# Performance work log

Hardware: AMD Instinct MI355X
Metric: run time of the kernel (lower is better)

The kernel has to match this reference:

```python
import jax, jax.numpy as jnp
import numpy as np

B, L, P, T, D, H = 16, 50, 49, 20, 512, 8
DH = D // H
DFF = 4 * D
EPS = 1e-6
NEG = -1000000000.0


def gelu_tanh(x):
    return 0.5 * x * (1.0 + jnp.tanh(jnp.sqrt(2.0 / jnp.pi) * (x + 0.044715 * x ** 3)))


def layernorm(x, a, b):
    # torch LayerNorm (custom): unbiased std, divide by (std + eps)
    mean = jnp.mean(x, axis=-1, keepdims=True)
    std = jnp.sqrt(jnp.var(x, axis=-1, keepdims=True, ddof=1))
    return a * (x - mean) / (std + EPS) + b


def setup_inputs() -> dict:
    key = jax.random.key(0)
    ks = jax.random.split(key, 20)
    s = 0.02
    return {
        "img": jax.random.normal(ks[0], (B, L, P, D), jnp.float32),
        "title": jax.random.normal(ks[1], (B, L, T, D), jnp.float32),
        "mask": jax.random.randint(ks[2], (B, L, T), 0, 2, jnp.int32),
        "scale_img": jax.random.normal(ks[3], (H, P), jnp.float32) * 0.1,
        "scale_title": jax.random.normal(ks[4], (H, T), jnp.float32) * 0.1,
        "w_proj": jax.random.normal(ks[5], (D, D), jnp.float32) * s,
        "b_proj": jnp.zeros((D,), jnp.float32),
        "w1_img": jax.random.normal(ks[6], (DFF, D), jnp.float32) * s,
        "b1_img": jnp.zeros((DFF,), jnp.float32),
        "w2_img": jax.random.normal(ks[7], (D, DFF), jnp.float32) * s,
        "b2_img": jnp.zeros((D,), jnp.float32),
        "w1_tit": jax.random.normal(ks[8], (DFF, D), jnp.float32) * s,
        "b1_tit": jnp.zeros((DFF,), jnp.float32),
        "w2_tit": jax.random.normal(ks[9], (D, DFF), jnp.float32) * s,
        "b2_tit": jnp.zeros((D,), jnp.float32),
        "ln_a_img": jnp.ones((D,), jnp.float32),
        "ln_b_img": jnp.zeros((D,), jnp.float32),
        "ln_a_tit": jnp.ones((D,), jnp.float32),
        "ln_b_tit": jnp.zeros((D,), jnp.float32),
    }


def _forward(img, title, mask, scale_img, scale_title, w_proj, b_proj,
             w1_img, b1_img, w2_img, b2_img, w1_tit, b1_tit, w2_tit, b2_tit,
             ln_a_img, ln_b_img, ln_a_tit, ln_b_tit):
    imgh = img.reshape(B, L, P, H, DH)      # [B,L,P,H,dh]
    tith = title.reshape(B, L, T, H, DH)    # [B,L,T,H,dh]

    raw = jnp.einsum('blphd,blthd->blhpt', imgh, tith) / jnp.sqrt(jnp.float32(DH))
    # corr_title is the transpose of the UNSCALED corr_img
    corr_img = raw * scale_img[None, None, :, :, None]                     # [B,L,H,P,T]
    corr_tit = jnp.swapaxes(raw, -1, -2) * scale_title[None, None, :, :, None]  # [B,L,H,T,P]

    m_img = mask[:, :, None, None, :]  # [B,L,1,1,T] -> broadcast over H,P
    m_tit = mask[:, :, None, :, None]  # [B,L,1,T,1]
    corr_img = jnp.where(m_img == 0, NEG, corr_img)
    corr_tit = jnp.where(m_tit == 0, NEG, corr_tit)

    p_img = jax.nn.softmax(corr_img, axis=-1)  # [B,L,H,P,T]
    p_tit = jax.nn.softmax(corr_tit, axis=-1)  # [B,L,H,T,P]

    # T != P, so the torch code takes the else branch (swapped outputs)
    hid_img = jnp.einsum('blhtp,blphd->blthd', p_tit, imgh).reshape(B, L, T, D)
    hid_tit = jnp.einsum('blhpt,blthd->blphd', p_img, tith).reshape(B, L, P, D)

    # both projected with img_layer (faithful to source)
    hid_img = hid_img @ w_proj.T + b_proj
    hid_tit = hid_tit @ w_proj.T + b_proj

    ffn_img = gelu_tanh(hid_img @ w1_img.T + b1_img) @ w2_img.T + b2_img
    ffn_tit = gelu_tanh(hid_tit @ w1_tit.T + b1_tit) @ w2_tit.T + b2_tit

    out_img = hid_img + layernorm(ffn_img, ln_a_img, ln_b_img)
    out_tit = hid_tit + layernorm(ffn_tit, ln_a_tit, ln_b_tit)
    return out_img, out_tit


def reference(img, title, mask, scale_img, scale_title, w_proj, b_proj,
              w1_img, b1_img, w2_img, b2_img, w1_tit, b1_tit, w2_tit, b2_tit,
              ln_a_img, ln_b_img, ln_a_tit, ln_b_tit):
    return _forward(img, title, mask, scale_img, scale_title, w_proj, b_proj,
                    w1_img, b1_img, w2_img, b2_img, w1_tit, b1_tit, w2_tit, b2_tit,
                    ln_a_img, ln_b_img, ln_a_tit, ln_b_tit)
```

## Files before the change

kernel.cpp:

```cpp
#include <hip/hip_runtime.h>
#include <hip/hip_bf16.h>

#define BB   16
#define LL   50
#define PP   49
#define TT   20
#define DD   512
#define HH   8
#define DHH  64
#define DFF  2048

#define BL     (BB*LL)
#define ROWS_I (BL*TT)
#define ROWS_T (BL*PP)
#define ROWS_A (ROWS_I+ROWS_T)
#define OUT_I_ELEMS ((size_t)ROWS_I*DD)
#define CHUNK 19600

#define R1_OFF 80281600ull
#define R2_OFF 136806400ull
#define R3_OFF 176947200ull

typedef __attribute__((ext_vector_type(8))) short bf16x8;
typedef __attribute__((ext_vector_type(4))) float f32x4;

__device__ __forceinline__ unsigned short f2bf(float f) {
    union { float f; unsigned int i; } w; w.f = f;
    unsigned int x = w.i;
    unsigned int r = (x + 0x7fffu + ((x >> 16) & 1u)) >> 16;
    return (unsigned short)r;
}
__device__ __forceinline__ float gelu_tanh_f(float x) {
    float c = 0.7978845608028654f * (x + 0.044715f * x * x * x);
    return 0.5f * x * (1.0f + tanhf(c));
}

__global__ __launch_bounds__(256) void cvt_kernel(
    const float* __restrict__ s, unsigned short* __restrict__ d, int n4)
{
    int i = blockIdx.x * 256 + threadIdx.x;
    if (i < n4) {
        float4 v = ((const float4*)s)[i];
        ushort4 u;
        u.x = f2bf(v.x); u.y = f2bf(v.y); u.z = f2bf(v.z); u.w = f2bf(v.w);
        ((ushort4*)d)[i] = u;
    }
}

__global__ __launch_bounds__(256) void attn_kernel(
    const float* __restrict__ img, const float* __restrict__ title,
    const int* __restrict__ mask, const float* __restrict__ scale_img,
    const float* __restrict__ scale_tit, unsigned short* __restrict__ hid)
{
    const int blh = blockIdx.x;
    const int h  = blh & 7;
    const int bl = blh >> 3;
    const int tid = threadIdx.x;

    __shared__ float simg[PP][DHH + 1];
    __shared__ float stit[TT][DHH + 1];
    __shared__ float S [PP][TT];
    __shared__ float pI[PP][TT];
    __shared__ float pT[TT][PP];
    __shared__ int   msk[TT];

    const float* imgbase = img   + (size_t)bl * PP * DD + h * DHH;
    const float* titbase = title + (size_t)bl * TT * DD + h * DHH;
    for (int i = tid; i < PP * DHH; i += 256) {
        int p = i >> 6, d = i & 63;
        simg[p][d] = imgbase[(size_t)p * DD + d];
    }
    for (int i = tid; i < TT * DHH; i += 256) {
        int t = i >> 6, d = i & 63;
        stit[t][d] = titbase[(size_t)t * DD + d];
    }
    if (tid < TT) msk[tid] = mask[bl * TT + tid];
    __syncthreads();

    for (int i = tid; i < PP * TT; i += 256) {
        int p = i / TT, t = i % TT;
        float s = 0.f;
        #pragma unroll 8
        for (int d = 0; d < DHH; ++d) s += simg[p][d] * stit[t][d];
        S[p][t] = s * 0.125f;
    }
    __syncthreads();

    if (tid < PP) {
        const int p = tid;
        const float sc = scale_img[h * PP + p];
        float m = -1e30f;
        #pragma unroll
        for (int t = 0; t < TT; ++t) {
            float x = (msk[t] == 0) ? -1e9f : S[p][t] * sc;
            m = fmaxf(m, x);
        }
        float sum = 0.f;
        #pragma unroll
        for (int t = 0; t < TT; ++t) {
            float x = (msk[t] == 0) ? -1e9f : S[p][t] * sc;
            float e = __expf(x - m);
            pI[p][t] = e; sum += e;
        }
        float inv = 1.f / sum;
        #pragma unroll
        for (int t = 0; t < TT; ++t) pI[p][t] *= inv;
    }
    if (tid >= 64 && tid < 64 + TT) {
        const int t = tid - 64;
        const float sc = scale_tit[h * TT + t];
        const bool dead = (msk[t] == 0);
        float m = -1e30f;
        #pragma unroll
        for (int p = 0; p < PP; ++p) {
            float x = dead ? -1e9f : S[p][t] * sc;
            m = fmaxf(m, x);
        }
        float sum = 0.f;
        #pragma unroll
        for (int p = 0; p < PP; ++p) {
            float x = dead ? -1e9f : S[p][t] * sc;
            float e = __expf(x - m);
            pT[t][p] = e; sum += e;
        }
        float inv = 1.f / sum;
        #pragma unroll
        for (int p = 0; p < PP; ++p) pT[t][p] *= inv;
    }
    __syncthreads();

    for (int i = tid; i < TT * DHH; i += 256) {
        int t = i >> 6, d = i & 63;
        float s = 0.f;
        #pragma unroll
        for (int p = 0; p < PP; ++p) s += pT[t][p] * simg[p][d];
        hid[(size_t)(bl * TT + t) * DD + h * DHH + d] = f2bf(s);
    }
    for (int i = tid; i < PP * DHH; i += 256) {
        int p = i >> 6, d = i & 63;
        float s = 0.f;
        #pragma unroll
        for (int t = 0; t < TT; ++t) s += pI[p][t] * stit[t][d];
        hid[OUT_I_ELEMS + (size_t)(bl * PP + p) * DD + h * DHH + d] = f2bf(s);
    }
}

template<bool GELU, bool F32OUT, bool BF16OUT>
__global__ __launch_bounds__(256) void gemm_mfma(
    const unsigned short* __restrict__ A, const unsigned short* __restrict__ Bw,
    const float* __restrict__ bias,
    float* __restrict__ Cf, unsigned short* __restrict__ Cb,
    int M, int N, int K)
{
    __shared__ unsigned short As[128 * 32];
    __shared__ unsigned short Bs[128 * 32];
    const int tid  = threadIdx.x;
    const int wave = tid >> 6;
    const int lane = tid & 63;
    const int row0 = blockIdx.y * 128;
    const int col0 = blockIdx.x * 128;
    const int m_off = (wave >> 1) * 64;
    const int n_off = (wave & 1) * 64;
    const int lane_m = lane & 15;
    const int lane_k = (lane >> 4) * 8;

    f32x4 acc[4][4] = {};

    for (int k0 = 0; k0 < K; k0 += 32) {
        #pragma unroll
        for (int q = 0; q < 2; ++q) {
            const int li = q * 256 + tid;
            int gr = row0 + (li >> 2);
            if (gr >= M) gr = M - 1;
            const unsigned short* gp = A + (size_t)gr * K + k0 + (li & 3) * 8;
            __builtin_amdgcn_global_load_lds(
                (const __attribute__((address_space(1))) unsigned int*)gp,
                (__attribute__((address_space(3))) unsigned int*)&As[li * 8], 16, 0, 0);
        }
        #pragma unroll
        for (int q = 0; q < 2; ++q) {
            const int li = q * 256 + tid;
            const unsigned short* gp = Bw + (size_t)(col0 + (li >> 2)) * K + k0 + (li & 3) * 8;
            __builtin_amdgcn_global_load_lds(
                (const __attribute__((address_space(1))) unsigned int*)gp,
                (__attribute__((address_space(3))) unsigned int*)&Bs[li * 8], 16, 0, 0);
        }
        __syncthreads();

        bf16x8 af[4], bf[4];
        #pragma unroll
        for (int i = 0; i < 4; ++i) {
            af[i] = *(const bf16x8*)&As[(m_off + i * 16 + lane_m) * 32 + lane_k];
            bf[i] = *(const bf16x8*)&Bs[(n_off + i * 16 + lane_m) * 32 + lane_k];
        }
        #pragma unroll
        for (int i = 0; i < 4; ++i)
            #pragma unroll
            for (int j = 0; j < 4; ++j)
                acc[i][j] = __builtin_amdgcn_mfma_f32_16x16x32_bf16(af[i], bf[j], acc[i][j], 0, 0, 0);
        __syncthreads();
    }

    #pragma unroll
    for (int i = 0; i < 4; ++i) {
        #pragma unroll
        for (int r = 0; r < 4; ++r) {
            const int row = row0 + m_off + i * 16 + (lane >> 4) * 4 + r;
            if (row < M) {
                #pragma unroll
                for (int j = 0; j < 4; ++j) {
                    const int col = col0 + n_off + j * 16 + lane_m;
                    float v = acc[i][j][r] + bias[col];
                    if (GELU) v = gelu_tanh_f(v);
                    if (F32OUT)  Cf[(size_t)row * N + col] = v;
                    if (BF16OUT) Cb[(size_t)row * N + col] = f2bf(v);
                }
            }
        }
    }
}

__global__ __launch_bounds__(256) void ln_res_kernel(
    const float* __restrict__ f2, float* __restrict__ out,
    const float* __restrict__ a, const float* __restrict__ b, int M)
{
    const int wave = threadIdx.x >> 6;
    const int lane = threadIdx.x & 63;
    const int row = blockIdx.x * 4 + wave;
    if (row >= M) return;
    const float* x = f2 + (size_t)row * DD;
    float* o = out + (size_t)row * DD;

    float xs[8];
    float s1 = 0.f, s2 = 0.f;
    #pragma unroll
    for (int i = 0; i < 8; ++i) {
        float v = x[lane + i * 64];
        xs[i] = v; s1 += v; s2 += v * v;
    }
    #pragma unroll
    for (int off = 32; off > 0; off >>= 1) {
        s1 += __shfl_xor(s1, off, 64);
        s2 += __shfl_xor(s2, off, 64);
    }
    const float mean = s1 * (1.f / 512.f);
    float var = (s2 - 512.f * mean * mean) * (1.f / 511.f);
    var = fmaxf(var, 0.f);
    const float rinv = 1.f / (sqrtf(var) + 1e-6f);
    #pragma unroll
    for (int i = 0; i < 8; ++i) {
        const int d = lane + i * 64;
        o[d] = o[d] + a[d] * (xs[i] - mean) * rinv + b[d];
    }
}

extern "C" void kernel_launch(void* const* d_in, const int* in_sizes, int n_in,
                              void* d_out, int out_size, void* d_ws, size_t ws_size,
                              hipStream_t stream) {
    const float* img       = (const float*)d_in[0];
    const float* title     = (const float*)d_in[1];
    const int*   mask      = (const int*)  d_in[2];
    const float* scale_img = (const float*)d_in[3];
    const float* scale_tit = (const float*)d_in[4];
    const float* w_proj    = (const float*)d_in[5];
    const float* b_proj    = (const float*)d_in[6];
    const float* w1_img    = (const float*)d_in[7];
    const float* b1_img    = (const float*)d_in[8];
    const float* w2_img    = (const float*)d_in[9];
    const float* b2_img    = (const float*)d_in[10];
    const float* w1_tit    = (const float*)d_in[11];
    const float* b1_tit    = (const float*)d_in[12];
    const float* w2_tit    = (const float*)d_in[13];
    const float* b2_tit    = (const float*)d_in[14];
    const float* ln_a_img  = (const float*)d_in[15];
    const float* ln_b_img  = (const float*)d_in[16];
    const float* ln_a_tit  = (const float*)d_in[17];
    const float* ln_b_tit  = (const float*)d_in[18];

    float* out = (float*)d_out;
    unsigned short* hid_bf = (unsigned short*)d_ws;
    unsigned short* act    = (unsigned short*)d_ws;
    unsigned short* out_bf = (unsigned short*)((char*)d_ws + R1_OFF);
    float*          f2     = (float*)((char*)d_ws + R2_OFF);
    unsigned short* wp_bf  = (unsigned short*)((char*)d_ws + R3_OFF);
    unsigned short* w1i_bf = wp_bf  + 262144;
    unsigned short* w2i_bf = w1i_bf + 1048576;
    unsigned short* w1t_bf = w2i_bf + 1048576;
    unsigned short* w2t_bf = w1t_bf + 1048576;

    cvt_kernel<<<(262144/4 + 255)/256, 256, 0, stream>>>(w_proj, wp_bf, 262144/4);
    cvt_kernel<<<(1048576/4 + 255)/256, 256, 0, stream>>>(w1_img, w1i_bf, 1048576/4);
    cvt_kernel<<<(1048576/4 + 255)/256, 256, 0, stream>>>(w2_img, w2i_bf, 1048576/4);
    cvt_kernel<<<(1048576/4 + 255)/256, 256, 0, stream>>>(w1_tit, w1t_bf, 1048576/4);
    cvt_kernel<<<(1048576/4 + 255)/256, 256, 0, stream>>>(w2_tit, w2t_bf, 1048576/4);

    attn_kernel<<<BL * HH, 256, 0, stream>>>(img, title, mask, scale_img, scale_tit, hid_bf);

    gemm_mfma<false, true, true><<<dim3(DD/128, (ROWS_A + 127)/128), 256, 0, stream>>>(
        hid_bf, wp_bf, b_proj, out, out_bf, ROWS_A, DD, DD);

    gemm_mfma<true, false, true><<<dim3(DFF/128, (ROWS_I + 127)/128), 256, 0, stream>>>(
        out_bf, w1i_bf, b1_img, nullptr, act, ROWS_I, DFF, DD);
    gemm_mfma<false, true, false><<<dim3(DD/128, (ROWS_I + 127)/128), 256, 0, stream>>>(
        act, w2i_bf, b2_img, f2, nullptr, ROWS_I, DD, DFF);
    ln_res_kernel<<<(ROWS_I + 3)/4, 256, 0, stream>>>(f2, out, ln_a_img, ln_b_img, ROWS_I);

    for (int c = 0; c < 2; ++c) {
        const unsigned short* a1 = out_bf + (size_t)(ROWS_I + c * CHUNK) * DD;
        float* o1 = out + OUT_I_ELEMS + (size_t)c * CHUNK * DD;
        gemm_mfma<true, false, true><<<dim3(DFF/128, (CHUNK + 127)/128), 256, 0, stream>>>(
            a1, w1t_bf, b1_tit, nullptr, act, CHUNK, DFF, DD);
        gemm_mfma<false, true, false><<<dim3(DD/128, (CHUNK + 127)/128), 256, 0, stream>>>(
            act, w2t_bf, b2_tit, f2, nullptr, CHUNK, DD, DFF);
        ln_res_kernel<<<(CHUNK + 3)/4, 256, 0, stream>>>(f2, o1, ln_a_tit, ln_b_tit, CHUNK);
    }
}
```

Measured before the change: 946.8 us.

## Vectorize attention kernel loads and register-tile score and output loops

Global-to-shared loads in the attention kernel now use float4, with shared rows padded to 68 floats. The score computation gives each thread four title rows, so every image-row load from shared memory is reused across four dot products. The two weighted-sum stages assign one output column per lane and one row group per wave, holding several accumulators in registers and reading probability rows as broadcast float4 loads. The goal is fewer shared-memory instructions and better load efficiency, at the cost of more registers and fewer active threads in the score stage (245 of 256).

```diff
diff --git a/kernel.cpp b/kernel.cpp
--- a/kernel.cpp
+++ b/kernel.cpp
@@ -56,33 +56,50 @@
     const int h  = blh & 7;
     const int bl = blh >> 3;
     const int tid = threadIdx.x;
-
-    __shared__ float simg[PP][DHH + 1];
-    __shared__ float stit[TT][DHH + 1];
-    __shared__ float S [PP][TT];
-    __shared__ float pI[PP][TT];
-    __shared__ float pT[TT][PP];
+    const int wave = tid >> 6;
+    const int lane = tid & 63;
+
+    __shared__ __align__(16) float simg[PP][68];
+    __shared__ __align__(16) float stit[TT][68];
+    __shared__ __align__(16) float S [PP][TT];
+    __shared__ __align__(16) float pI[PP][TT];
+    __shared__ __align__(16) float pT[TT][52];
     __shared__ int   msk[TT];
 
     const float* imgbase = img   + (size_t)bl * PP * DD + h * DHH;
     const float* titbase = title + (size_t)bl * TT * DD + h * DHH;
-    for (int i = tid; i < PP * DHH; i += 256) {
-        int p = i >> 6, d = i & 63;
-        simg[p][d] = imgbase[(size_t)p * DD + d];
-    }
-    for (int i = tid; i < TT * DHH; i += 256) {
-        int t = i >> 6, d = i & 63;
-        stit[t][d] = titbase[(size_t)t * DD + d];
+
+    for (int i = tid; i < PP * 16; i += 256) {
+        int p = i >> 4, d4 = i & 15;
+        *(float4*)&simg[p][d4 * 4] = *(const float4*)(imgbase + (size_t)p * DD + d4 * 4);
+    }
+    for (int i = tid; i < TT * 16; i += 256) {
+        int t = i >> 4, d4 = i & 15;
+        *(float4*)&stit[t][d4 * 4] = *(const float4*)(titbase + (size_t)t * DD + d4 * 4);
     }
     if (tid < TT) msk[tid] = mask[bl * TT + tid];
     __syncthreads();
 
-    for (int i = tid; i < PP * TT; i += 256) {
-        int p = i / TT, t = i % TT;
-        float s = 0.f;
-        #pragma unroll 8
-        for (int d = 0; d < DHH; ++d) s += simg[p][d] * stit[t][d];
-        S[p][t] = s * 0.125f;
+    if (tid < PP * 5) {
+        const int p  = tid / 5;
+        const int tg = tid - p * 5;
+        float a0 = 0.f, a1 = 0.f, a2 = 0.f, a3 = 0.f;
+        #pragma unroll 4
+        for (int d = 0; d < DHH; d += 4) {
+            float4 a  = *(const float4*)&simg[p][d];
+            float4 b0 = *(const float4*)&stit[tg     ][d];
+            float4 b1 = *(const float4*)&stit[tg +  5][d];
+            float4 b2 = *(const float4*)&stit[tg + 10][d];
+            float4 b3 = *(const float4*)&stit[tg + 15][d];
+            a0 += a.x*b0.x + a.y*b0.y + a.z*b0.z + a.w*b0.w;
+            a1 += a.x*b1.x + a.y*b1.y + a.z*b1.z + a.w*b1.w;
+            a2 += a.x*b2.x + a.y*b2.y + a.z*b2.z + a.w*b2.w;
+            a3 += a.x*b3.x + a.y*b3.y + a.z*b3.z + a.w*b3.w;
+        }
+        S[p][tg     ] = a0 * 0.125f;
+        S[p][tg +  5] = a1 * 0.125f;
+        S[p][tg + 10] = a2 * 0.125f;
+        S[p][tg + 15] = a3 * 0.125f;
     }
     __syncthreads();
 
@@ -129,19 +146,57 @@
     }
     __syncthreads();
 
-    for (int i = tid; i < TT * DHH; i += 256) {
-        int t = i >> 6, d = i & 63;
-        float s = 0.f;
-        #pragma unroll
-        for (int p = 0; p < PP; ++p) s += pT[t][p] * simg[p][d];
-        hid[(size_t)(bl * TT + t) * DD + h * DHH + d] = f2bf(s);
-    }
-    for (int i = tid; i < PP * DHH; i += 256) {
-        int p = i >> 6, d = i & 63;
-        float s = 0.f;
-        #pragma unroll
-        for (int t = 0; t < TT; ++t) s += pI[p][t] * stit[t][d];
-        hid[OUT_I_ELEMS + (size_t)(bl * PP + p) * DD + h * DHH + d] = f2bf(s);
+    {
+        float accA[5] = {0.f, 0.f, 0.f, 0.f, 0.f};
+        #pragma unroll
+        for (int p = 0; p < 48; p += 4) {
+            float v0 = simg[p + 0][lane];
+            float v1 = simg[p + 1][lane];
+            float v2 = simg[p + 2][lane];
+            float v3 = simg[p + 3][lane];
+            #pragma unroll
+            for (int j = 0; j < 5; ++j) {
+                const int t = wave + j * 4;
+                float4 w4 = *(const float4*)&pT[t][p];
+                accA[j] += v0 * w4.x + v1 * w4.y + v2 * w4.z + v3 * w4.w;
+            }
+        }
+        {
+            float v0 = simg[48][lane];
+            #pragma unroll
+            for (int j = 0; j < 5; ++j)
+                accA[j] += v0 * pT[wave + j * 4][48];
+        }
+        #pragma unroll
+        for (int j = 0; j < 5; ++j) {
+            const int t = wave + j * 4;
+            hid[(size_t)(bl * TT + t) * DD + h * DHH + lane] = f2bf(accA[j]);
+        }
+    }
+
+    {
+        float accB[13] = {0.f,0.f,0.f,0.f,0.f,0.f,0.f,0.f,0.f,0.f,0.f,0.f,0.f};
+        #pragma unroll
+        for (int t = 0; t < TT; t += 4) {
+            float v0 = stit[t + 0][lane];
+            float v1 = stit[t + 1][lane];
+            float v2 = stit[t + 2][lane];
+            float v3 = stit[t + 3][lane];
+            #pragma unroll
+            for (int j = 0; j < 13; ++j) {
+                const int p = wave + j * 4;
+                if (p < PP) {
+                    float4 w4 = *(const float4*)&pI[p][t];
+                    accB[j] += v0 * w4.x + v1 * w4.y + v2 * w4.z + v3 * w4.w;
+                }
+            }
+        }
+        #pragma unroll
+        for (int j = 0; j < 13; ++j) {
+            const int p = wave + j * 4;
+            if (p < PP)
+                hid[OUT_I_ELEMS + (size_t)(bl * PP + p) * DD + h * DHH + lane] = f2bf(accB[j]);
+        }
     }
 }
 
```

Measured after the change: 906.1 us. -4.3%, faster.
